# Kernel optimization log

Measured on AMD Instinct MI355X. Metric: run time of the kernel, lower is better.

The kernel has to match this reference:

```python
import jax, jax.numpy as jnp
import numpy as np

K = 10  # value-iteration steps


def _conv(x, w):
    # NCHW x OIHW -> NCHW, stride 1, SAME padding (pad=2 for 5x5, pad=0 for 1x1)
    return jax.lax.conv_general_dilated(
        x, w, window_strides=(1, 1), padding='SAME',
        dimension_numbers=('NCHW', 'OIHW', 'NCHW'))


def setup_inputs() -> dict:
    key = jax.random.key(0)
    ks = jax.random.split(key, 6)
    B, H, W = 64, 64, 64
    dim_h, n_hat, n_act = 150, 8, 4
    maze = jax.random.randint(ks[0], (B, H, W), 0, 3)
    # fixed embedding table from the torch module
    emb = jnp.array([[0.0, 0.0], [1.0, 0.0], [0.0, 10.0]], dtype=jnp.float32)
    encode_w = jax.random.normal(ks[1], (dim_h, 2, 5, 5), dtype=jnp.float32) * 0.05
    encode_b = jnp.zeros((dim_h,), dtype=jnp.float32)
    r_w = jax.random.normal(ks[2], (1, dim_h, 1, 1), dtype=jnp.float32) * 0.05
    q_w = jax.random.normal(ks[3], (n_hat, 1, 5, 5), dtype=jnp.float32) * 0.05
    # torch inits self.w to zeros; use small randn so the recurrence is non-trivial
    w = jax.random.normal(ks[4], (n_hat, 1, 5, 5), dtype=jnp.float32) * 0.05
    fc_w = jax.random.normal(ks[5], (n_act, n_hat), dtype=jnp.float32) * 0.1
    return dict(maze=maze, emb=emb, encode_w=encode_w, encode_b=encode_b,
                r_w=r_w, q_w=q_w, w=w, fc_w=fc_w)


def reference(maze, emb, encode_w, encode_b, r_w, q_w, w, fc_w):
    # embed: [B,H,W] -> [B,H,W,2] -> [B,2,H,W]
    m = emb[maze].transpose(0, 3, 1, 2)
    h = _conv(m, encode_w) + encode_b[None, :, None, None]  # [B,150,H,W]
    r = _conv(h, r_w)                                        # [B,1,H,W]
    q = _conv(r, q_w)                                        # [B,8,H,W]
    wk = jnp.concatenate([q_w, w], axis=1)                   # [8,2,5,5]

    def step(q, _):
        v = jnp.max(q, axis=1, keepdims=True)                # [B,1,H,W]
        q = _conv(jnp.concatenate([r, v], axis=1), wk)       # [B,8,H,W]
        return q, None

    q, _ = jax.lax.scan(step, q, None, length=K)
    q = q.transpose(0, 2, 3, 1)                              # [B,H,W,8]
    return q @ fc_w.T                                        # [B,H,W,4]
```

## Files before the change

### kernel.cpp

```cpp
#include <hip/hip_runtime.h>
#include <hip/hip_bf16.h>


#define NHAT 8
#define DIMH 150

typedef float v2f __attribute__((ext_vector_type(2)));

__global__ __launch_bounds__(512) void rq_kernel(
    const int* __restrict__ maze, const float* __restrict__ emb,
    const float* __restrict__ encode_w, const float* __restrict__ encode_b,
    const float* __restrict__ r_w, const float* __restrict__ q_w,
    float* __restrict__ q0g) {
  __shared__ float wpart[5][50];
  __shared__ float bpart[152];
  __shared__ float weff[2][25];
  __shared__ float Ts[4][25];
  __shared__ float bsh;
  __shared__ v2f qw2[25][4];
  __shared__ unsigned char mzt[24][68];
  __shared__ float rt[20][68];

  int tid = threadIdx.x;
  int b = blockIdx.y, A0 = blockIdx.x * 16;

  if (tid < 100) {
    int k = tid >> 2, j = tid & 3;
    qw2[k][j] = (v2f){q_w[(2 * j) * 25 + k], q_w[(2 * j + 1) * 25 + k]};
  }
  if (tid >= 256 && tid < 506) {
    int t2 = tid - 256;
    int chunk = t2 / 50, ik = t2 % 50;
    int i = ik / 25, k = ik % 25;
    int c0 = chunk * 30;
    float s = 0.f;
    for (int c = c0; c < c0 + 30; ++c)
      s += r_w[c] * encode_w[c * 50 + i * 25 + k];
    wpart[chunk][ik] = s;
  }
  if (tid >= 100 && tid < 250) {
    int c = tid - 100;
    bpart[c] = r_w[c] * encode_b[c];
  }
  for (int i = tid; i < 24 * 68; i += 512) {
    int mr = i / 68, mc = i % 68;
    int gy = A0 - 4 + mr, gx = mc - 2;
    unsigned char v = 3;
    if (gy >= 0 && gy < 64 && gx >= 0 && gx < 64)
      v = (unsigned char)maze[(b * 64 + gy) * 64 + gx];
    mzt[mr][mc] = v;
  }
  __syncthreads();
  if (tid < 50) {
    float s = 0.f;
#pragma unroll
    for (int ch = 0; ch < 5; ++ch) s += wpart[ch][tid];
    weff[tid / 25][tid % 25] = s;
  }
  if (tid == 50) {
    float s = 0.f;
    for (int c = 0; c < 150; ++c) s += bpart[c];
    bsh = s;
  }
  __syncthreads();
  if (tid < 100) {
    int val = tid / 25, k = tid % 25;
    float t = 0.f;
    if (val < 3) t = weff[0][k] * emb[val * 2] + weff[1][k] * emb[val * 2 + 1];
    Ts[val][k] = t;
  }
  __syncthreads();
  for (int i = tid; i < 20 * 68; i += 512) {
    int rr = i / 68, cc = i % 68;
    int gy = A0 - 2 + rr, gx = cc - 2;
    float v = 0.f;
    if (gy >= 0 && gy < 64 && gx >= 0 && gx < 64) {
      v = bsh;
#pragma unroll
      for (int ky = 0; ky < 5; ++ky)
#pragma unroll
        for (int kx = 0; kx < 5; ++kx)
          v += Ts[mzt[rr + ky][cc - 2 + kx]][ky * 5 + kx];
    }
    rt[rr][cc] = v;
  }
  __syncthreads();
  for (int i = tid; i < 16 * 64; i += 512) {
    int ly = i >> 6, gx = i & 63;
    int gy = A0 + ly;
    v2f acc[4];
#pragma unroll
    for (int j = 0; j < 4; ++j) acc[j] = (v2f){0.f, 0.f};
#pragma unroll
    for (int ky = 0; ky < 5; ++ky)
#pragma unroll
      for (int kx = 0; kx < 5; ++kx) {
        int k = ky * 5 + kx;
        float vv = rt[ly + ky][gx + kx];
        v2f vv2 = (v2f){vv, vv};
#pragma unroll
        for (int j = 0; j < 4; ++j) acc[j] += qw2[k][j] * vv2;
      }
#pragma unroll
    for (int j = 0; j < 4; ++j)
      *(v2f*)&q0g[(((size_t)(b * 64 + gy) * 4 + j) * 64 + gx) * 2] = acc[j];
  }
}

__global__ __launch_bounds__(1024, 4) void vi_kernel(
    const float* __restrict__ q0g, const float* __restrict__ w,
    const float* __restrict__ fc_w, float* __restrict__ out) {
  __shared__ __align__(16) float vbuf[2][60][68];
  __shared__ v2f wl2[25][4];

  int tid = threadIdx.x;
  int b = blockIdx.y, a0 = blockIdx.x * 16;
  int wave = tid >> 6, lane = tid & 63;
  int cq = lane >> 4;
  int p4 = (lane & 15) * 4;

  if (tid < 100) {
    int k = tid >> 2, j = tid & 3;
    wl2[k][j] = (v2f){w[(2 * j) * 25 + k], w[(2 * j + 1) * 25 + k]};
  }
  for (int i = tid; i < 2 * 60 * 68; i += 1024) ((float*)vbuf)[i] = 0.f;
  __syncthreads();

  v2f wr[25];
#pragma unroll
  for (int k = 0; k < 25; ++k) wr[k] = wl2[k][cq];

  const float* q0b = q0g + (size_t)b * 64 * 4 * 64 * 2;
  int cur = 0;

  {
    int s = max(0, a0 - 20), e = min(64, a0 + 36);
    int gx = lane;
    for (int r = s + wave; r < e; r += 16) {
      v2f a0v = *(const v2f*)&q0b[(((size_t)r * 4 + 0) * 64 + gx) * 2];
      v2f a1v = *(const v2f*)&q0b[(((size_t)r * 4 + 1) * 64 + gx) * 2];
      v2f a2v = *(const v2f*)&q0b[(((size_t)r * 4 + 2) * 64 + gx) * 2];
      v2f a3v = *(const v2f*)&q0b[(((size_t)r * 4 + 3) * 64 + gx) * 2];
      float m = fmaxf(fmaxf(fmaxf(a0v.x, a0v.y), fmaxf(a1v.x, a1v.y)),
                      fmaxf(fmaxf(a2v.x, a2v.y), fmaxf(a3v.x, a3v.y)));
      vbuf[0][r - a0 + 22][gx + 2] = m;
    }
  }
  __syncthreads();

  for (int t = 1; t <= 9; ++t) {
    int hh = 2 * (10 - t);
    int s = max(0, a0 - hh), e = min(64, a0 + 16 + hh);
    for (int r = s + wave; r < e; r += 16) {
      int lr = r - a0 + 22;
      const float4* qp =
          (const float4*)&q0b[(((size_t)r * 4 + cq) * 64 + p4) * 2];
      float4 qv0 = qp[0], qv1 = qp[1];
      v2f aA[4];
#pragma unroll
      for (int j = 0; j < 4; ++j) aA[j] = (v2f){0.f, 0.f};
#pragma unroll
      for (int jj = 0; jj < 5; ++jj) {
        const float* row = &vbuf[cur][lr - 2 + jj][p4];
        float4 fa = *(const float4*)row;
        float4 fb = *(const float4*)(row + 4);
        float f[8] = {fa.x, fa.y, fa.z, fa.w, fb.x, fb.y, fb.z, fb.w};
#pragma unroll
        for (int kx = 0; kx < 5; ++kx) {
          v2f wk = wr[jj * 5 + kx];
#pragma unroll
          for (int j = 0; j < 4; ++j) {
            v2f vv2 = (v2f){f[j + kx], f[j + kx]};
            aA[j] += wk * vv2;
          }
        }
      }
      aA[0] += (v2f){qv0.x, qv0.y};
      aA[1] += (v2f){qv0.z, qv0.w};
      aA[2] += (v2f){qv1.x, qv1.y};
      aA[3] += (v2f){qv1.z, qv1.w};
      float m0 = fmaxf(aA[0].x, aA[0].y), m1 = fmaxf(aA[1].x, aA[1].y);
      float m2 = fmaxf(aA[2].x, aA[2].y), m3 = fmaxf(aA[3].x, aA[3].y);
      m0 = fmaxf(m0, __shfl_xor(m0, 16)); m0 = fmaxf(m0, __shfl_xor(m0, 32));
      m1 = fmaxf(m1, __shfl_xor(m1, 16)); m1 = fmaxf(m1, __shfl_xor(m1, 32));
      m2 = fmaxf(m2, __shfl_xor(m2, 16)); m2 = fmaxf(m2, __shfl_xor(m2, 32));
      m3 = fmaxf(m3, __shfl_xor(m3, 16)); m3 = fmaxf(m3, __shfl_xor(m3, 32));
      if (cq == 0) {
        *(v2f*)&vbuf[cur ^ 1][lr][2 + p4] = (v2f){m0, m1};
        *(v2f*)&vbuf[cur ^ 1][lr][4 + p4] = (v2f){m2, m3};
      }
    }
    __syncthreads();
    cur ^= 1;
  }

  {
    int r = a0 + wave;
    int lr = r - a0 + 22;
    const float4* qp =
        (const float4*)&q0b[(((size_t)r * 4 + cq) * 64 + p4) * 2];
    float4 qv0 = qp[0], qv1 = qp[1];
    v2f aA[4];
#pragma unroll
    for (int j = 0; j < 4; ++j) aA[j] = (v2f){0.f, 0.f};
#pragma unroll
    for (int jj = 0; jj < 5; ++jj) {
      const float* row = &vbuf[cur][lr - 2 + jj][p4];
      float4 fa = *(const float4*)row;
      float4 fb = *(const float4*)(row + 4);
      float f[8] = {fa.x, fa.y, fa.z, fa.w, fb.x, fb.y, fb.z, fb.w};
#pragma unroll
      for (int kx = 0; kx < 5; ++kx) {
        v2f wk = wr[jj * 5 + kx];
#pragma unroll
        for (int j = 0; j < 4; ++j) {
          v2f vv2 = (v2f){f[j + kx], f[j + kx]};
          aA[j] += wk * vv2;
        }
      }
    }
    aA[0] += (v2f){qv0.x, qv0.y};
    aA[1] += (v2f){qv0.z, qv0.w};
    aA[2] += (v2f){qv1.x, qv1.y};
    aA[3] += (v2f){qv1.z, qv1.w};
    v2f fcp2[4];
#pragma unroll
    for (int a = 0; a < 4; ++a)
      fcp2[a] = (v2f){fc_w[a * 8 + 2 * cq], fc_w[a * 8 + 2 * cq + 1]};
#pragma unroll
    for (int j = 0; j < 4; ++j) {
      float p0 = fcp2[0].x * aA[j].x + fcp2[0].y * aA[j].y;
      float p1 = fcp2[1].x * aA[j].x + fcp2[1].y * aA[j].y;
      float p2 = fcp2[2].x * aA[j].x + fcp2[2].y * aA[j].y;
      float p3 = fcp2[3].x * aA[j].x + fcp2[3].y * aA[j].y;
      p0 += __shfl_xor(p0, 16); p0 += __shfl_xor(p0, 32);
      p1 += __shfl_xor(p1, 16); p1 += __shfl_xor(p1, 32);
      p2 += __shfl_xor(p2, 16); p2 += __shfl_xor(p2, 32);
      p3 += __shfl_xor(p3, 16); p3 += __shfl_xor(p3, 32);
      if (cq == 0)
        *(float4*)&out[((size_t)((b * 64 + r) * 64 + p4 + j)) * 4] =
            make_float4(p0, p1, p2, p3);
    }
  }
}

extern "C" void kernel_launch(void* const* d_in, const int* in_sizes, int n_in,
                              void* d_out, int out_size, void* d_ws, size_t ws_size,
                              hipStream_t stream) {
  const int* maze = (const int*)d_in[0];
  const float* emb = (const float*)d_in[1];
  const float* encode_w = (const float*)d_in[2];
  const float* encode_b = (const float*)d_in[3];
  const float* r_w = (const float*)d_in[4];
  const float* q_w = (const float*)d_in[5];
  const float* w = (const float*)d_in[6];
  const float* fc_w = (const float*)d_in[7];
  float* out = (float*)d_out;

  float* q0g = (float*)d_ws;

  rq_kernel<<<dim3(4, 64), 512, 0, stream>>>(maze, emb, encode_w, encode_b,
                                             r_w, q_w, q0g);
  vi_kernel<<<dim3(4, 64), 1024, 0, stream>>>(q0g, w, fc_w, out);
}
```

Baseline: 115.3 us.

## Switch q0 workspace to channel-planar layout and map one channel per lane group

Rewrites the q0 intermediate from a channel-pair interleaved layout to a per-channel row-planar layout, and remaps value-iteration lanes so each group of 8 lanes handles one channel over 8 consecutive columns. Each lane now packs two adjacent pixels with one broadcast weight into a v2f FMA, instead of two channels with one broadcast pixel. This doubles the pixels per lane, adding a third LDS float4 load per row and an extra shuffle stage for the channel max. It also changes the rq kernel's stores to scalar strided writes and reworks the final fc projection.

```diff
diff --git a/kernel.cpp b/kernel.cpp
--- a/kernel.cpp
+++ b/kernel.cpp
@@ -101,9 +101,12 @@
 #pragma unroll
         for (int j = 0; j < 4; ++j) acc[j] += qw2[k][j] * vv2;
       }
-#pragma unroll
-    for (int j = 0; j < 4; ++j)
-      *(v2f*)&q0g[(((size_t)(b * 64 + gy) * 4 + j) * 64 + gx) * 2] = acc[j];
+    size_t base = ((size_t)(b * 64 + gy) * 8) * 64 + gx;
+#pragma unroll
+    for (int j = 0; j < 4; ++j) {
+      q0g[base + (size_t)(2 * j) * 64] = acc[j].x;
+      q0g[base + (size_t)(2 * j + 1) * 64] = acc[j].y;
+    }
   }
 }
 
@@ -111,38 +114,36 @@
     const float* __restrict__ q0g, const float* __restrict__ w,
     const float* __restrict__ fc_w, float* __restrict__ out) {
   __shared__ __align__(16) float vbuf[2][60][68];
-  __shared__ v2f wl2[25][4];
+  __shared__ float wl[25][8];
 
   int tid = threadIdx.x;
   int b = blockIdx.y, a0 = blockIdx.x * 16;
   int wave = tid >> 6, lane = tid & 63;
-  int cq = lane >> 4;
-  int p4 = (lane & 15) * 4;
-
-  if (tid < 100) {
-    int k = tid >> 2, j = tid & 3;
-    wl2[k][j] = (v2f){w[(2 * j) * 25 + k], w[(2 * j + 1) * 25 + k]};
+  int ch = lane >> 3;
+  int p8 = (lane & 7) * 8;
+
+  if (tid < 200) {
+    int k = tid >> 3, c = tid & 7;
+    wl[k][c] = w[c * 25 + k];
   }
   for (int i = tid; i < 2 * 60 * 68; i += 1024) ((float*)vbuf)[i] = 0.f;
   __syncthreads();
 
-  v2f wr[25];
-#pragma unroll
-  for (int k = 0; k < 25; ++k) wr[k] = wl2[k][cq];
-
-  const float* q0b = q0g + (size_t)b * 64 * 4 * 64 * 2;
+  float wr[25];
+#pragma unroll
+  for (int k = 0; k < 25; ++k) wr[k] = wl[k][ch];
+
+  const float* q0b = q0g + (size_t)b * 64 * 8 * 64;
   int cur = 0;
 
   {
     int s = max(0, a0 - 20), e = min(64, a0 + 36);
     int gx = lane;
     for (int r = s + wave; r < e; r += 16) {
-      v2f a0v = *(const v2f*)&q0b[(((size_t)r * 4 + 0) * 64 + gx) * 2];
-      v2f a1v = *(const v2f*)&q0b[(((size_t)r * 4 + 1) * 64 + gx) * 2];
-      v2f a2v = *(const v2f*)&q0b[(((size_t)r * 4 + 2) * 64 + gx) * 2];
-      v2f a3v = *(const v2f*)&q0b[(((size_t)r * 4 + 3) * 64 + gx) * 2];
-      float m = fmaxf(fmaxf(fmaxf(a0v.x, a0v.y), fmaxf(a1v.x, a1v.y)),
-                      fmaxf(fmaxf(a2v.x, a2v.y), fmaxf(a3v.x, a3v.y)));
+      const float* qr = &q0b[((size_t)r * 8) * 64 + gx];
+      float m = qr[0];
+#pragma unroll
+      for (int c = 1; c < 8; ++c) m = fmaxf(m, qr[(size_t)c * 64]);
       vbuf[0][r - a0 + 22][gx + 2] = m;
     }
   }
@@ -153,41 +154,48 @@
     int s = max(0, a0 - hh), e = min(64, a0 + 16 + hh);
     for (int r = s + wave; r < e; r += 16) {
       int lr = r - a0 + 22;
-      const float4* qp =
-          (const float4*)&q0b[(((size_t)r * 4 + cq) * 64 + p4) * 2];
-      float4 qv0 = qp[0], qv1 = qp[1];
-      v2f aA[4];
-#pragma unroll
-      for (int j = 0; j < 4; ++j) aA[j] = (v2f){0.f, 0.f};
+      const float* qrow = &q0b[((size_t)r * 8 + ch) * 64 + p8];
+      float4 qa = *(const float4*)qrow;
+      float4 qb = *(const float4*)(qrow + 4);
+      v2f acc[4];
+#pragma unroll
+      for (int j = 0; j < 4; ++j) acc[j] = (v2f){0.f, 0.f};
 #pragma unroll
       for (int jj = 0; jj < 5; ++jj) {
-        const float* row = &vbuf[cur][lr - 2 + jj][p4];
+        const float* row = &vbuf[cur][lr - 2 + jj][p8];
         float4 fa = *(const float4*)row;
         float4 fb = *(const float4*)(row + 4);
-        float f[8] = {fa.x, fa.y, fa.z, fa.w, fb.x, fb.y, fb.z, fb.w};
+        float4 fc = *(const float4*)(row + 8);
+        float f[12] = {fa.x, fa.y, fa.z, fa.w, fb.x, fb.y,
+                       fb.z, fb.w, fc.x, fc.y, fc.z, fc.w};
 #pragma unroll
         for (int kx = 0; kx < 5; ++kx) {
-          v2f wk = wr[jj * 5 + kx];
-#pragma unroll
-          for (int j = 0; j < 4; ++j) {
-            v2f vv2 = (v2f){f[j + kx], f[j + kx]};
-            aA[j] += wk * vv2;
-          }
+          float wk = wr[jj * 5 + kx];
+          v2f wk2 = (v2f){wk, wk};
+#pragma unroll
+          for (int j = 0; j < 4; ++j)
+            acc[j] += wk2 * (v2f){f[2 * j + kx], f[2 * j + 1 + kx]};
         }
       }
-      aA[0] += (v2f){qv0.x, qv0.y};
-      aA[1] += (v2f){qv0.z, qv0.w};
-      aA[2] += (v2f){qv1.x, qv1.y};
-      aA[3] += (v2f){qv1.z, qv1.w};
-      float m0 = fmaxf(aA[0].x, aA[0].y), m1 = fmaxf(aA[1].x, aA[1].y);
-      float m2 = fmaxf(aA[2].x, aA[2].y), m3 = fmaxf(aA[3].x, aA[3].y);
-      m0 = fmaxf(m0, __shfl_xor(m0, 16)); m0 = fmaxf(m0, __shfl_xor(m0, 32));
-      m1 = fmaxf(m1, __shfl_xor(m1, 16)); m1 = fmaxf(m1, __shfl_xor(m1, 32));
-      m2 = fmaxf(m2, __shfl_xor(m2, 16)); m2 = fmaxf(m2, __shfl_xor(m2, 32));
-      m3 = fmaxf(m3, __shfl_xor(m3, 16)); m3 = fmaxf(m3, __shfl_xor(m3, 32));
-      if (cq == 0) {
-        *(v2f*)&vbuf[cur ^ 1][lr][2 + p4] = (v2f){m0, m1};
-        *(v2f*)&vbuf[cur ^ 1][lr][4 + p4] = (v2f){m2, m3};
+      acc[0] += (v2f){qa.x, qa.y};
+      acc[1] += (v2f){qa.z, qa.w};
+      acc[2] += (v2f){qb.x, qb.y};
+      acc[3] += (v2f){qb.z, qb.w};
+      float m0 = acc[0].x, m1 = acc[0].y, m2 = acc[1].x, m3 = acc[1].y;
+      float m4 = acc[2].x, m5 = acc[2].y, m6 = acc[3].x, m7 = acc[3].y;
+      m0 = fmaxf(m0, __shfl_xor(m0, 8));  m0 = fmaxf(m0, __shfl_xor(m0, 16));  m0 = fmaxf(m0, __shfl_xor(m0, 32));
+      m1 = fmaxf(m1, __shfl_xor(m1, 8));  m1 = fmaxf(m1, __shfl_xor(m1, 16));  m1 = fmaxf(m1, __shfl_xor(m1, 32));
+      m2 = fmaxf(m2, __shfl_xor(m2, 8));  m2 = fmaxf(m2, __shfl_xor(m2, 16));  m2 = fmaxf(m2, __shfl_xor(m2, 32));
+      m3 = fmaxf(m3, __shfl_xor(m3, 8));  m3 = fmaxf(m3, __shfl_xor(m3, 16));  m3 = fmaxf(m3, __shfl_xor(m3, 32));
+      m4 = fmaxf(m4, __shfl_xor(m4, 8));  m4 = fmaxf(m4, __shfl_xor(m4, 16));  m4 = fmaxf(m4, __shfl_xor(m4, 32));
+      m5 = fmaxf(m5, __shfl_xor(m5, 8));  m5 = fmaxf(m5, __shfl_xor(m5, 16));  m5 = fmaxf(m5, __shfl_xor(m5, 32));
+      m6 = fmaxf(m6, __shfl_xor(m6, 8));  m6 = fmaxf(m6, __shfl_xor(m6, 16));  m6 = fmaxf(m6, __shfl_xor(m6, 32));
+      m7 = fmaxf(m7, __shfl_xor(m7, 8));  m7 = fmaxf(m7, __shfl_xor(m7, 16));  m7 = fmaxf(m7, __shfl_xor(m7, 32));
+      if (ch == 0) {
+        *(v2f*)&vbuf[cur ^ 1][lr][2 + p8] = (v2f){m0, m1};
+        *(v2f*)&vbuf[cur ^ 1][lr][4 + p8] = (v2f){m2, m3};
+        *(v2f*)&vbuf[cur ^ 1][lr][6 + p8] = (v2f){m4, m5};
+        *(v2f*)&vbuf[cur ^ 1][lr][8 + p8] = (v2f){m6, m7};
       }
     }
     __syncthreads();
@@ -197,48 +205,50 @@
   {
     int r = a0 + wave;
     int lr = r - a0 + 22;
-    const float4* qp =
-        (const float4*)&q0b[(((size_t)r * 4 + cq) * 64 + p4) * 2];
-    float4 qv0 = qp[0], qv1 = qp[1];
-    v2f aA[4];
-#pragma unroll
-    for (int j = 0; j < 4; ++j) aA[j] = (v2f){0.f, 0.f};
+    const float* qrow = &q0b[((size_t)r * 8 + ch) * 64 + p8];
+    float4 qa = *(const float4*)qrow;
+    float4 qb = *(const float4*)(qrow + 4);
+    v2f acc[4];
+#pragma unroll
+    for (int j = 0; j < 4; ++j) acc[j] = (v2f){0.f, 0.f};
 #pragma unroll
     for (int jj = 0; jj < 5; ++jj) {
-      const float* row = &vbuf[cur][lr - 2 + jj][p4];
+      const float* row = &vbuf[cur][lr - 2 + jj][p8];
       float4 fa = *(const float4*)row;
       float4 fb = *(const float4*)(row + 4);
-      float f[8] = {fa.x, fa.y, fa.z, fa.w, fb.x, fb.y, fb.z, fb.w};
+      float4 fc = *(const float4*)(row + 8);
+      float f[12] = {fa.x, fa.y, fa.z, fa.w, fb.x, fb.y,
+                     fb.z, fb.w, fc.x, fc.y, fc.z, fc.w};
 #pragma unroll
       for (int kx = 0; kx < 5; ++kx) {
-        v2f wk = wr[jj * 5 + kx];
-#pragma unroll
-        for (int j = 0; j < 4; ++j) {
-          v2f vv2 = (v2f){f[j + kx], f[j + kx]};
-          aA[j] += wk * vv2;
-        }
-      }
-    }
-    aA[0] += (v2f){qv0.x, qv0.y};
-    aA[1] += (v2f){qv0.z, qv0.w};
-    aA[2] += (v2f){qv1.x, qv1.y};
-    aA[3] += (v2f){qv1.z, qv1.w};
-    v2f fcp2[4];
-#pragma unroll
-    for (int a = 0; a < 4; ++a)
-      fcp2[a] = (v2f){fc_w[a * 8 + 2 * cq], fc_w[a * 8 + 2 * cq + 1]};
-#pragma unroll
-    for (int j = 0; j < 4; ++j) {
-      float p0 = fcp2[0].x * aA[j].x + fcp2[0].y * aA[j].y;
-      float p1 = fcp2[1].x * aA[j].x + fcp2[1].y * aA[j].y;
-      float p2 = fcp2[2].x * aA[j].x + fcp2[2].y * aA[j].y;
-      float p3 = fcp2[3].x * aA[j].x + fcp2[3].y * aA[j].y;
-      p0 += __shfl_xor(p0, 16); p0 += __shfl_xor(p0, 32);
-      p1 += __shfl_xor(p1, 16); p1 += __shfl_xor(p1, 32);
-      p2 += __shfl_xor(p2, 16); p2 += __shfl_xor(p2, 32);
-      p3 += __shfl_xor(p3, 16); p3 += __shfl_xor(p3, 32);
-      if (cq == 0)
-        *(float4*)&out[((size_t)((b * 64 + r) * 64 + p4 + j)) * 4] =
+        float wk = wr[jj * 5 + kx];
+        v2f wk2 = (v2f){wk, wk};
+#pragma unroll
+        for (int j = 0; j < 4; ++j)
+          acc[j] += wk2 * (v2f){f[2 * j + kx], f[2 * j + 1 + kx]};
+      }
+    }
+    acc[0] += (v2f){qa.x, qa.y};
+    acc[1] += (v2f){qa.z, qa.w};
+    acc[2] += (v2f){qb.x, qb.y};
+    acc[3] += (v2f){qb.z, qb.w};
+    float fcp[4];
+#pragma unroll
+    for (int a = 0; a < 4; ++a) fcp[a] = fc_w[a * 8 + ch];
+    float qv[8] = {acc[0].x, acc[0].y, acc[1].x, acc[1].y,
+                   acc[2].x, acc[2].y, acc[3].x, acc[3].y};
+#pragma unroll
+    for (int i = 0; i < 8; ++i) {
+      float p0 = fcp[0] * qv[i];
+      float p1 = fcp[1] * qv[i];
+      float p2 = fcp[2] * qv[i];
+      float p3 = fcp[3] * qv[i];
+      p0 += __shfl_xor(p0, 8); p0 += __shfl_xor(p0, 16); p0 += __shfl_xor(p0, 32);
+      p1 += __shfl_xor(p1, 8); p1 += __shfl_xor(p1, 16); p1 += __shfl_xor(p1, 32);
+      p2 += __shfl_xor(p2, 8); p2 += __shfl_xor(p2, 16); p2 += __shfl_xor(p2, 32);
+      p3 += __shfl_xor(p3, 8); p3 += __shfl_xor(p3, 16); p3 += __shfl_xor(p3, 32);
+      if (ch == 0)
+        *(float4*)&out[((size_t)((b * 64 + r) * 64 + p8 + i)) * 4] =
             make_float4(p0, p1, p2, p3);
     }
   }
```

Measured after the change: 145.5 us. 1.26x slower.
